# Kernel optimization log

Measured on AMD Instinct MI355X. Metric: run time of the kernel, lower is better.

The kernel has to match this reference:

```python
import jax, jax.numpy as jnp
import numpy as np

D_MODEL = 1024
NHEAD = 16
D_K = D_MODEL // NHEAD


def sparsemax(z):
    # sparsemax along last axis (Martins & Astudillo 2016)
    n = z.shape[-1]
    z_sorted = jnp.flip(jnp.sort(z, axis=-1), axis=-1)          # descending
    k = jnp.arange(1, n + 1, dtype=z.dtype)
    z_cumsum = jnp.cumsum(z_sorted, axis=-1)
    support = (1.0 + k * z_sorted) > z_cumsum                    # [..., n] bool
    k_max = jnp.sum(support, axis=-1, keepdims=True)             # [..., 1] int
    tau_sum = jnp.take_along_axis(z_cumsum, k_max - 1, axis=-1)
    tau = (tau_sum - 1.0) / k_max.astype(z.dtype)
    return jnp.maximum(z - tau, 0.0)


def setup_inputs() -> dict:
    key = jax.random.key(0)
    ks = jax.random.split(key, 12)
    B, S = 2, 2048
    s = 1.0 / np.sqrt(D_MODEL)
    inp = {
        'query': jax.random.normal(ks[0], (B, S, D_MODEL), jnp.float32),
        'key':   jax.random.normal(ks[1], (B, S, D_MODEL), jnp.float32),
        'value': jax.random.normal(ks[2], (B, S, D_MODEL), jnp.float32),
        'Wq': jax.random.uniform(ks[3], (D_MODEL, D_MODEL), jnp.float32, -s, s),
        'bq': jax.random.uniform(ks[4], (D_MODEL,), jnp.float32, -s, s),
        'Wk': jax.random.uniform(ks[5], (D_MODEL, D_MODEL), jnp.float32, -s, s),
        'bk': jax.random.uniform(ks[6], (D_MODEL,), jnp.float32, -s, s),
        'Wv': jax.random.uniform(ks[7], (D_MODEL, D_MODEL), jnp.float32, -s, s),
        'bv': jax.random.uniform(ks[8], (D_MODEL,), jnp.float32, -s, s),
        'Wfc': jax.random.uniform(ks[9], (D_MODEL, D_MODEL), jnp.float32, -s, s),
        'bfc': jax.random.uniform(ks[10], (D_MODEL,), jnp.float32, -s, s),
    }
    return inp


def reference(query, key, value, Wq, bq, Wk, bk, Wv, bv, Wfc, bfc):
    B, S, _ = query.shape
    # projections (torch Linear: x @ W.T + b)
    q = (query @ Wq.T + bq).reshape(B, S, NHEAD, D_K).transpose(0, 2, 1, 3)
    k = (key   @ Wk.T + bk).reshape(B, S, NHEAD, D_K).transpose(0, 2, 1, 3)
    v = (value @ Wv.T + bv).reshape(B, S, NHEAD, D_K).transpose(0, 2, 1, 3)
    # scaled dot-product with sparsemax
    logits = jnp.einsum('bhqd,bhkd->bhqk', q, k) / np.sqrt(D_K).astype(jnp.float32)
    attention = sparsemax(logits)                                # [B,H,S,S]
    attn_out = jnp.einsum('bhqk,bhkd->bhqd', attention, v)
    attn_out = attn_out.transpose(0, 2, 1, 3).reshape(B, S, D_MODEL)
    output = attn_out @ Wfc.T + bfc                              # dropout = identity (eval)
    return output, attention
```

## Files before the change

### kernel.cpp

```cpp
#include <hip/hip_runtime.h>
#include <hip/hip_bf16.h>
#include <cstdint>

#define S_LEN  2048
#define DMODEL 1024
#define NHEAD  16
#define M_ROWS 4096

typedef __attribute__((ext_vector_type(8))) short bf16x8;
typedef __attribute__((ext_vector_type(4))) float f32x4;

__device__ __forceinline__ unsigned short f2bf(float f) {
    __hip_bfloat16 h = __float2bfloat16(f);
    return __builtin_bit_cast(unsigned short, h);
}
__device__ __forceinline__ float bf2f(unsigned short u) {
    return __builtin_bit_cast(float, (unsigned)u << 16);
}
__device__ __forceinline__ uint4 pack8(float4 a, float4 b) {
    uint4 u;
    u.x = ((unsigned)f2bf(a.y) << 16) | f2bf(a.x);
    u.y = ((unsigned)f2bf(a.w) << 16) | f2bf(a.z);
    u.z = ((unsigned)f2bf(b.y) << 16) | f2bf(b.x);
    u.w = ((unsigned)f2bf(b.w) << 16) | f2bf(b.z);
    return u;
}

__device__ __forceinline__ float wave_sum64(float v) {
    v += __shfl_xor(v, 32, 64); v += __shfl_xor(v, 16, 64);
    v += __shfl_xor(v, 8, 64);  v += __shfl_xor(v, 4, 64);
    v += __shfl_xor(v, 2, 64);  v += __shfl_xor(v, 1, 64);
    return v;
}
__device__ __forceinline__ float wave_max64(float v) {
    v = fmaxf(v, __shfl_xor(v, 32, 64)); v = fmaxf(v, __shfl_xor(v, 16, 64));
    v = fmaxf(v, __shfl_xor(v, 8, 64));  v = fmaxf(v, __shfl_xor(v, 4, 64));
    v = fmaxf(v, __shfl_xor(v, 2, 64));  v = fmaxf(v, __shfl_xor(v, 1, 64));
    return v;
}
__device__ __forceinline__ int lanes_below(unsigned long long m) {
    return __builtin_amdgcn_mbcnt_hi((unsigned)(m >> 32),
           __builtin_amdgcn_mbcnt_lo((unsigned)m, 0));
}

__global__ __launch_bounds__(256)
void qkv_gemm(const float* __restrict__ xq, const float* __restrict__ xk,
              const float* __restrict__ xv,
              const float* __restrict__ Wq, const float* __restrict__ Wk,
              const float* __restrict__ Wv,
              const float* __restrict__ bq, const float* __restrict__ bk,
              const float* __restrict__ bv,
              unsigned short* __restrict__ Q_bf, unsigned short* __restrict__ K_bf,
              unsigned short* __restrict__ V_bf) {
    const int which = blockIdx.z;
    const float* A    = (which == 0) ? xq : (which == 1) ? xk : xv;
    const float* W    = (which == 0) ? Wq : (which == 1) ? Wk : Wv;
    const float* bias = (which == 0) ? bq : (which == 1) ? bk : bv;
    unsigned short* dst = (which == 0) ? Q_bf : (which == 1) ? K_bf : V_bf;

    const int row0 = blockIdx.x * 128;
    const int col0 = blockIdx.y * 128;

    __shared__ unsigned short SMEM[10240];
    unsigned short* As = SMEM;
    unsigned short* Bs = SMEM + 5120;

    const int t = threadIdx.x;
    const int wid = t >> 6, lane = t & 63;
    const int wm = wid >> 1, wn = wid & 1;
    const int l = lane & 15, quad = lane >> 4;

    f32x4 acc[4][4];
#pragma unroll
    for (int i = 0; i < 4; ++i)
#pragma unroll
        for (int j = 0; j < 4; ++j) {
            float b_ = bias[col0 + wn * 64 + j * 16 + l];
            acc[i][j] = (f32x4){ b_, b_, b_, b_ };
        }

    for (int k0 = 0; k0 < DMODEL; k0 += 32) {
        uint4 ar[2], br[2];
#pragma unroll
        for (int i = 0; i < 2; ++i) {
            const int c = t + i * 256, r = c >> 2, q = (c & 3) * 8;
            const float* ap = A + (size_t)(row0 + r) * DMODEL + k0 + q;
            const float* wp = W + (size_t)(col0 + r) * DMODEL + k0 + q;
            float4 a0 = *(const float4*)ap, a1 = *(const float4*)(ap + 4);
            float4 w0 = *(const float4*)wp, w1 = *(const float4*)(wp + 4);
            ar[i] = pack8(a0, a1);
            br[i] = pack8(w0, w1);
        }
        __syncthreads();
#pragma unroll
        for (int i = 0; i < 2; ++i) {
            const int c = t + i * 256, r = c >> 2, q = (c & 3) * 8;
            *(uint4*)&As[r * 40 + q] = ar[i];
            *(uint4*)&Bs[r * 40 + q] = br[i];
        }
        __syncthreads();
        bf16x8 a[4], b[4];
#pragma unroll
        for (int i = 0; i < 4; ++i)
            a[i] = *(const bf16x8*)&As[(wm * 64 + i * 16 + l) * 40 + quad * 8];
#pragma unroll
        for (int j = 0; j < 4; ++j)
            b[j] = *(const bf16x8*)&Bs[(wn * 64 + j * 16 + l) * 40 + quad * 8];
#pragma unroll
        for (int i = 0; i < 4; ++i)
#pragma unroll
            for (int j = 0; j < 4; ++j)
                acc[i][j] = __builtin_amdgcn_mfma_f32_16x16x32_bf16(a[i], b[j], acc[i][j], 0, 0, 0);
    }

    __syncthreads();
    unsigned short* Cs = SMEM;
#pragma unroll 1
    for (int jh = 0; jh < 2; ++jh) {
        if (wn == jh) {
#pragma unroll
            for (int i = 0; i < 4; ++i)
#pragma unroll
                for (int j = 0; j < 4; ++j)
#pragma unroll
                    for (int r = 0; r < 4; ++r)
                        Cs[(wm * 64 + i * 16 + quad * 4 + r) * 72 + j * 16 + l] =
                            f2bf(acc[i][j][r]);
        }
        __syncthreads();
#pragma unroll
        for (int it = 0; it < 4; ++it) {
            const int idx = t + it * 256;
            const int row = idx >> 3, c8 = (idx & 7) * 8;
            *(uint4*)(dst + (size_t)(row0 + row) * DMODEL + col0 + jh * 64 + c8) =
                *(const uint4*)&Cs[row * 72 + c8];
        }
        __syncthreads();
    }
}

__global__ __launch_bounds__(512, 8)
void attn_fused(const unsigned short* __restrict__ Q_bf,
                const unsigned short* __restrict__ K_bf,
                const unsigned short* __restrict__ V_bf,
                float* __restrict__ attn,
                unsigned short* __restrict__ AO_bf) {
    const int t = threadIdx.x;
    const int w = t >> 6, lane = t & 63;
    const int l = lane & 15, quad = lane >> 4;
    const int bh = blockIdx.y, b_ = bh >> 4, h = bh & 15;
    const int r0 = blockIdx.x * 8;

    __shared__ float LDSf[8 * 512];

    const unsigned short* Qp =
        Q_bf + ((size_t)(b_ * S_LEN + r0 + (l & 7))) * DMODEL + h * 64 + quad * 8;
    const bf16x8 a0 = *(const bf16x8*)Qp;
    const bf16x8 a1 = *(const bf16x8*)(Qp + 32);

    float z[32];
#pragma unroll
    for (int q = 0; q < 4; ++q) {
        const unsigned short* Kb =
            K_bf + ((size_t)(b_ * S_LEN + q * 512 + w * 64 + l)) * DMODEL
            + h * 64 + quad * 8;
        f32x4 acc[4];
#pragma unroll
        for (int ct = 0; ct < 4; ++ct) {
            const unsigned short* Kp = Kb + (size_t)(ct * 16) * DMODEL;
            const bf16x8 b0 = *(const bf16x8*)Kp;
            const bf16x8 b1 = *(const bf16x8*)(Kp + 32);
            f32x4 c = {};
            c = __builtin_amdgcn_mfma_f32_16x16x32_bf16(a0, b0, c, 0, 0, 0);
            c = __builtin_amdgcn_mfma_f32_16x16x32_bf16(a1, b1, c, 0, 0, 0);
#pragma unroll
            for (int r = 0; r < 4; ++r) c[r] *= 0.125f;
            acc[ct] = c;
        }
        if (quad < 2) {
#pragma unroll
            for (int ct = 0; ct < 4; ++ct)
#pragma unroll
                for (int r = 0; r < 4; ++r)
                    LDSf[(quad * 4 + r) * 512 + w * 64 + ct * 16 + l] = acc[ct][r];
        }
        __syncthreads();
#pragma unroll
        for (int j = 0; j < 8; ++j)
            z[q * 8 + j] = LDSf[w * 512 + j * 64 + lane];
        __syncthreads();
    }

    float m = z[0];
#pragma unroll
    for (int j = 1; j < 32; ++j) m = fmaxf(m, z[j]);
    m = wave_max64(m);

    float tau = m - 1.0f;
#pragma unroll 1
    for (int it = 0; it < 8; ++it) {
        float ss = 0.0f, kk = 0.0f;
#pragma unroll
        for (int j = 0; j < 32; ++j)
            if (z[j] > tau) { ss += z[j]; kk += 1.0f; }
        ss = wave_sum64(ss); kk = wave_sum64(kk);
        const float tn = (ss - 1.0f) / kk;
        if (tn == tau) break;
        tau = tn;
    }

    float* ap = attn + (size_t)bh * S_LEN * S_LEN + (size_t)(r0 + w) * S_LEN;
#pragma unroll
    for (int jj = 0; jj < 32; ++jj) {
        z[jj] = fmaxf(z[jj] - tau, 0.0f);
        __builtin_nontemporal_store(z[jj], ap + (jj >> 3) * 512 + (jj & 7) * 64 + lane);
    }

    uint2* list = (uint2*)LDSf + w * 256;
    int base = 0;
#pragma unroll
    for (int jj = 0; jj < 32; ++jj) {
        const float pv = z[jj];
        const unsigned long long mk = __ballot(pv > 0.0f);
        if (pv > 0.0f) {
            const int pos = base + lanes_below(mk);
            if (pos < 256)
                list[pos] = (uint2){ (unsigned)((jj >> 3) * 512 + (jj & 7) * 64 + lane),
                                     __builtin_bit_cast(unsigned, pv) };
        }
        base += __popcll(mk);
    }
    const int cnt = base < 256 ? base : 256;
    __threadfence_block();

    const unsigned short* Vh = V_bf + ((size_t)b_ * S_LEN) * DMODEL + h * 64;
    const int sub = lane >> 3, dbase = (lane & 7) * 8;
    float acc8[8] = {};
    const int gmax = (cnt + 7) >> 3;
#pragma unroll 1
    for (int g = 0; g < gmax; ++g) {
        const int idx = g * 8 + sub;
        if (idx < cnt) {
            const uint2 e = list[idx];
            const float p = __builtin_bit_cast(float, e.y);
            const uint4 vv = *(const uint4*)(Vh + ((size_t)e.x) * DMODEL + dbase);
            acc8[0] += p * bf2f((unsigned short)(vv.x & 0xffff));
            acc8[1] += p * bf2f((unsigned short)(vv.x >> 16));
            acc8[2] += p * bf2f((unsigned short)(vv.y & 0xffff));
            acc8[3] += p * bf2f((unsigned short)(vv.y >> 16));
            acc8[4] += p * bf2f((unsigned short)(vv.z & 0xffff));
            acc8[5] += p * bf2f((unsigned short)(vv.z >> 16));
            acc8[6] += p * bf2f((unsigned short)(vv.w & 0xffff));
            acc8[7] += p * bf2f((unsigned short)(vv.w >> 16));
        }
    }
#pragma unroll
    for (int d = 0; d < 8; ++d) {
        acc8[d] += __shfl_xor(acc8[d], 8, 64);
        acc8[d] += __shfl_xor(acc8[d], 16, 64);
        acc8[d] += __shfl_xor(acc8[d], 32, 64);
    }
    if (lane < 8) {
        union { unsigned short u[8]; uint4 v; } o;
#pragma unroll
        for (int d = 0; d < 8; ++d) o.u[d] = f2bf(acc8[d]);
        *(uint4*)(AO_bf + ((size_t)(b_ * S_LEN + r0 + w)) * DMODEL
                  + h * 64 + lane * 8) = o.v;
    }
}

__global__ __launch_bounds__(256)
void fc_gemm(const unsigned short* __restrict__ AO_bf,
             const float* __restrict__ Wfc,
             const float* __restrict__ bfc, float* __restrict__ out) {
    const int row0 = blockIdx.x * 128;
    const int col0 = blockIdx.y * 128;

    __shared__ unsigned short As[128 * 40];
    __shared__ unsigned short Bs[128 * 40];

    const int t = threadIdx.x;
    const int wid = t >> 6, lane = t & 63;
    const int wm = wid >> 1, wn = wid & 1;
    const int l = lane & 15, quad = lane >> 4;

    f32x4 acc[4][4];
#pragma unroll
    for (int i = 0; i < 4; ++i)
#pragma unroll
        for (int j = 0; j < 4; ++j) {
            float b_ = bfc[col0 + wn * 64 + j * 16 + l];
            acc[i][j] = (f32x4){ b_, b_, b_, b_ };
        }

    for (int k0 = 0; k0 < DMODEL; k0 += 32) {
        uint4 ar[2], br[2];
#pragma unroll
        for (int i = 0; i < 2; ++i) {
            const int c = t + i * 256, r = c >> 2, q = (c & 3) * 8;
            ar[i] = *(const uint4*)(AO_bf + (size_t)(row0 + r) * DMODEL + k0 + q);
            const float* wp = Wfc + (size_t)(col0 + r) * DMODEL + k0 + q;
            float4 w0 = *(const float4*)wp, w1 = *(const float4*)(wp + 4);
            br[i] = pack8(w0, w1);
        }
        __syncthreads();
#pragma unroll
        for (int i = 0; i < 2; ++i) {
            const int c = t + i * 256, r = c >> 2, q = (c & 3) * 8;
            *(uint4*)&As[r * 40 + q] = ar[i];
            *(uint4*)&Bs[r * 40 + q] = br[i];
        }
        __syncthreads();
        bf16x8 a[4], b[4];
#pragma unroll
        for (int i = 0; i < 4; ++i)
            a[i] = *(const bf16x8*)&As[(wm * 64 + i * 16 + l) * 40 + quad * 8];
#pragma unroll
        for (int j = 0; j < 4; ++j)
            b[j] = *(const bf16x8*)&Bs[(wn * 64 + j * 16 + l) * 40 + quad * 8];
#pragma unroll
        for (int i = 0; i < 4; ++i)
#pragma unroll
            for (int j = 0; j < 4; ++j)
                acc[i][j] = __builtin_amdgcn_mfma_f32_16x16x32_bf16(a[i], b[j], acc[i][j], 0, 0, 0);
    }

#pragma unroll
    for (int i = 0; i < 4; ++i)
#pragma unroll
        for (int r = 0; r < 4; ++r) {
            const int m = row0 + wm * 64 + i * 16 + quad * 4 + r;
#pragma unroll
            for (int j = 0; j < 4; ++j) {
                const int n = col0 + wn * 64 + j * 16 + l;
                out[(size_t)m * DMODEL + n] = acc[i][j][r];
            }
        }
}

extern "C" void kernel_launch(void* const* d_in, const int* in_sizes, int n_in,
                              void* d_out, int out_size, void* d_ws, size_t ws_size,
                              hipStream_t stream) {
    const float* q   = (const float*)d_in[0];
    const float* k   = (const float*)d_in[1];
    const float* v   = (const float*)d_in[2];
    const float* Wq  = (const float*)d_in[3];
    const float* bq  = (const float*)d_in[4];
    const float* Wk  = (const float*)d_in[5];
    const float* bk  = (const float*)d_in[6];
    const float* Wv  = (const float*)d_in[7];
    const float* bv  = (const float*)d_in[8];
    const float* Wfc = (const float*)d_in[9];
    const float* bfc = (const float*)d_in[10];

    float* out  = (float*)d_out;
    float* attn = out + (size_t)M_ROWS * DMODEL;

    char* ws = (char*)d_ws;
    unsigned short* Q_bf  = (unsigned short*)ws;
    unsigned short* K_bf  = (unsigned short*)(ws + (8u << 20));
    unsigned short* V_bf  = (unsigned short*)(ws + (16u << 20));
    unsigned short* AO_bf = (unsigned short*)(ws + (24u << 20));

    qkv_gemm<<<dim3(32, 8, 3), 256, 0, stream>>>(q, k, v, Wq, Wk, Wv,
                                                  bq, bk, bv, Q_bf, K_bf, V_bf);
    attn_fused<<<dim3(S_LEN / 8, 32), 512, 0, stream>>>(Q_bf, K_bf, V_bf, attn, AO_bf);
    fc_gemm<<<dim3(32, 8), 256, 0, stream>>>(AO_bf, Wfc, bfc, out);
}
```

Baseline: 906.6 us.

## Prefilter sparsemax candidates above max-1 and fold Q scaling into projection

Result: no change. 906.3 us (-0.0%).

```diff
diff --git a/kernel.cpp b/kernel.cpp
--- a/kernel.cpp
+++ b/kernel.cpp
@@ -57,6 +57,7 @@
     const float* W    = (which == 0) ? Wq : (which == 1) ? Wk : Wv;
     const float* bias = (which == 0) ? bq : (which == 1) ? bk : bv;
     unsigned short* dst = (which == 0) ? Q_bf : (which == 1) ? K_bf : V_bf;
+    const float qscale = (which == 0) ? 0.125f : 1.0f;
 
     const int row0 = blockIdx.x * 128;
     const int col0 = blockIdx.y * 128;
@@ -125,7 +126,7 @@
 #pragma unroll
                     for (int r = 0; r < 4; ++r)
                         Cs[(wm * 64 + i * 16 + quad * 4 + r) * 72 + j * 16 + l] =
-                            f2bf(acc[i][j][r]);
+                            f2bf(acc[i][j][r] * qscale);
         }
         __syncthreads();
 #pragma unroll
@@ -151,7 +152,8 @@
     const int bh = blockIdx.y, b_ = bh >> 4, h = bh & 15;
     const int r0 = blockIdx.x * 8;
 
-    __shared__ float LDSf[8 * 512];
+    __shared__ uint2 List[8 * 512];
+    float* LDSf = (float*)List;
 
     const unsigned short* Qp =
         Q_bf + ((size_t)(b_ * S_LEN + r0 + (l & 7))) * DMODEL + h * 64 + quad * 8;
@@ -173,8 +175,6 @@
             f32x4 c = {};
             c = __builtin_amdgcn_mfma_f32_16x16x32_bf16(a0, b0, c, 0, 0, 0);
             c = __builtin_amdgcn_mfma_f32_16x16x32_bf16(a1, b1, c, 0, 0, 0);
-#pragma unroll
-            for (int r = 0; r < 4; ++r) c[r] *= 0.125f;
             acc[ct] = c;
         }
         if (quad < 2) {
@@ -195,64 +195,104 @@
 #pragma unroll
     for (int j = 1; j < 32; ++j) m = fmaxf(m, z[j]);
     m = wave_max64(m);
-
-    float tau = m - 1.0f;
+    const float thr = m - 1.0f;
+
+    uint2* list = List + w * 512;
+    int cnt = 0;
+#pragma unroll
+    for (int jj = 0; jj < 32; ++jj) {
+        const float zv = z[jj];
+        const unsigned long long mk = __ballot(zv > thr);
+        if (zv > thr) {
+            const int pos = cnt + lanes_below(mk);
+            if (pos < 512)
+                list[pos] = (uint2){ (unsigned)((jj >> 3) * 512 + (jj & 7) * 64 + lane),
+                                     __builtin_bit_cast(unsigned, zv) };
+        }
+        cnt += __popcll(mk);
+    }
+    __threadfence_block();
+
+    float tau = thr;
+    if (cnt <= 256) {
+        const float NEG = -__builtin_inff();
+        const float zc0 = (lane < cnt)
+            ? __builtin_bit_cast(float, list[lane].y) : NEG;
+        const float zc1 = (64 + lane < cnt)
+            ? __builtin_bit_cast(float, list[64 + lane].y) : NEG;
+        const float zc2 = (128 + lane < cnt)
+            ? __builtin_bit_cast(float, list[128 + lane].y) : NEG;
+        const float zc3 = (192 + lane < cnt)
+            ? __builtin_bit_cast(float, list[192 + lane].y) : NEG;
 #pragma unroll 1
-    for (int it = 0; it < 8; ++it) {
-        float ss = 0.0f, kk = 0.0f;
-#pragma unroll
-        for (int j = 0; j < 32; ++j)
-            if (z[j] > tau) { ss += z[j]; kk += 1.0f; }
-        ss = wave_sum64(ss); kk = wave_sum64(kk);
-        const float tn = (ss - 1.0f) / kk;
-        if (tn == tau) break;
-        tau = tn;
-    }
+        for (int it = 0; it < 12; ++it) {
+            float ss = 0.0f, kk = 0.0f;
+            if (zc0 > tau) { ss += zc0; kk += 1.0f; }
+            if (zc1 > tau) { ss += zc1; kk += 1.0f; }
+            if (zc2 > tau) { ss += zc2; kk += 1.0f; }
+            if (zc3 > tau) { ss += zc3; kk += 1.0f; }
+            ss = wave_sum64(ss); kk = wave_sum64(kk);
+            const float tn = (ss - 1.0f) / kk;
+            if (tn == tau) break;
+            tau = tn;
+        }
+    } else {
+#pragma unroll 1
+        for (int it = 0; it < 8; ++it) {
+            float ss = 0.0f, kk = 0.0f;
+#pragma unroll
+            for (int j = 0; j < 32; ++j)
+                if (z[j] > tau) { ss += z[j]; kk += 1.0f; }
+            ss = wave_sum64(ss); kk = wave_sum64(kk);
+            const float tn = (ss - 1.0f) / kk;
+            if (tn == tau) break;
+            tau = tn;
+        }
+        cnt = 0;
+#pragma unroll
+        for (int jj = 0; jj < 32; ++jj) {
+            const float zv = z[jj];
+            const unsigned long long mk = __ballot(zv > tau);
+            if (zv > tau) {
+                const int pos = cnt + lanes_below(mk);
+                if (pos < 512)
+                    list[pos] = (uint2){ (unsigned)((jj >> 3) * 512 + (jj & 7) * 64 + lane),
+                                         __builtin_bit_cast(unsigned, zv) };
+            }
+            cnt += __popcll(mk);
+        }
+        __threadfence_block();
+    }
+    if (cnt > 504) cnt = 504;
 
     float* ap = attn + (size_t)bh * S_LEN * S_LEN + (size_t)(r0 + w) * S_LEN;
 #pragma unroll
     for (int jj = 0; jj < 32; ++jj) {
-        z[jj] = fmaxf(z[jj] - tau, 0.0f);
-        __builtin_nontemporal_store(z[jj], ap + (jj >> 3) * 512 + (jj & 7) * 64 + lane);
-    }
-
-    uint2* list = (uint2*)LDSf + w * 256;
-    int base = 0;
-#pragma unroll
-    for (int jj = 0; jj < 32; ++jj) {
-        const float pv = z[jj];
-        const unsigned long long mk = __ballot(pv > 0.0f);
-        if (pv > 0.0f) {
-            const int pos = base + lanes_below(mk);
-            if (pos < 256)
-                list[pos] = (uint2){ (unsigned)((jj >> 3) * 512 + (jj & 7) * 64 + lane),
-                                     __builtin_bit_cast(unsigned, pv) };
-        }
-        base += __popcll(mk);
-    }
-    const int cnt = base < 256 ? base : 256;
+        const float pv = fmaxf(z[jj] - tau, 0.0f);
+        __builtin_nontemporal_store(pv, ap + (jj >> 3) * 512 + (jj & 7) * 64 + lane);
+    }
+
+    if (lane < 8)
+        list[cnt + lane] = (uint2){ 0u, 0xff800000u };
     __threadfence_block();
 
     const unsigned short* Vh = V_bf + ((size_t)b_ * S_LEN) * DMODEL + h * 64;
     const int sub = lane >> 3, dbase = (lane & 7) * 8;
     float acc8[8] = {};
     const int gmax = (cnt + 7) >> 3;
-#pragma unroll 1
+#pragma unroll 2
     for (int g = 0; g < gmax; ++g) {
-        const int idx = g * 8 + sub;
-        if (idx < cnt) {
-            const uint2 e = list[idx];
-            const float p = __builtin_bit_cast(float, e.y);
-            const uint4 vv = *(const uint4*)(Vh + ((size_t)e.x) * DMODEL + dbase);
-            acc8[0] += p * bf2f((unsigned short)(vv.x & 0xffff));
-            acc8[1] += p * bf2f((unsigned short)(vv.x >> 16));
-            acc8[2] += p * bf2f((unsigned short)(vv.y & 0xffff));
-            acc8[3] += p * bf2f((unsigned short)(vv.y >> 16));
-            acc8[4] += p * bf2f((unsigned short)(vv.z & 0xffff));
-            acc8[5] += p * bf2f((unsigned short)(vv.z >> 16));
-            acc8[6] += p * bf2f((unsigned short)(vv.w & 0xffff));
-            acc8[7] += p * bf2f((unsigned short)(vv.w >> 16));
-        }
+        const uint2 e = list[g * 8 + sub];
+        const float p = fmaxf(__builtin_bit_cast(float, e.y) - tau, 0.0f);
+        const uint4 vv = *(const uint4*)(Vh + ((size_t)e.x) * DMODEL + dbase);
+        acc8[0] += p * bf2f((unsigned short)(vv.x & 0xffff));
+        acc8[1] += p * bf2f((unsigned short)(vv.x >> 16));
+        acc8[2] += p * bf2f((unsigned short)(vv.y & 0xffff));
+        acc8[3] += p * bf2f((unsigned short)(vv.y >> 16));
+        acc8[4] += p * bf2f((unsigned short)(vv.z & 0xffff));
+        acc8[5] += p * bf2f((unsigned short)(vv.z >> 16));
+        acc8[6] += p * bf2f((unsigned short)(vv.w & 0xffff));
+        acc8[7] += p * bf2f((unsigned short)(vv.w >> 16));
     }
 #pragma unroll
     for (int d = 0; d < 8; ++d) {
```

## Fold Q scaling into projection, unroll sparse PV gather, enlarge support list

Applied to the files above, without the earlier changes.

Measured after the change: 890.3 us. Within noise of the previous version (-1.8%).

```diff
diff --git a/kernel.cpp b/kernel.cpp
--- a/kernel.cpp
+++ b/kernel.cpp
@@ -57,6 +57,7 @@
     const float* W    = (which == 0) ? Wq : (which == 1) ? Wk : Wv;
     const float* bias = (which == 0) ? bq : (which == 1) ? bk : bv;
     unsigned short* dst = (which == 0) ? Q_bf : (which == 1) ? K_bf : V_bf;
+    const float qscale = (which == 0) ? 0.125f : 1.0f;
 
     const int row0 = blockIdx.x * 128;
     const int col0 = blockIdx.y * 128;
@@ -125,7 +126,7 @@
 #pragma unroll
                     for (int r = 0; r < 4; ++r)
                         Cs[(wm * 64 + i * 16 + quad * 4 + r) * 72 + j * 16 + l] =
-                            f2bf(acc[i][j][r]);
+                            f2bf(acc[i][j][r] * qscale);
         }
         __syncthreads();
 #pragma unroll
@@ -139,7 +140,7 @@
     }
 }
 
-__global__ __launch_bounds__(512, 8)
+__global__ __launch_bounds__(512, 6)
 void attn_fused(const unsigned short* __restrict__ Q_bf,
                 const unsigned short* __restrict__ K_bf,
                 const unsigned short* __restrict__ V_bf,
@@ -151,7 +152,8 @@
     const int bh = blockIdx.y, b_ = bh >> 4, h = bh & 15;
     const int r0 = blockIdx.x * 8;
 
-    __shared__ float LDSf[8 * 512];
+    __shared__ uint2 List[8 * 512];
+    float* LDSf = (float*)List;
 
     const unsigned short* Qp =
         Q_bf + ((size_t)(b_ * S_LEN + r0 + (l & 7))) * DMODEL + h * 64 + quad * 8;
@@ -159,6 +161,7 @@
     const bf16x8 a1 = *(const bf16x8*)(Qp + 32);
 
     float z[32];
+    float m = -__builtin_inff();
 #pragma unroll
     for (int q = 0; q < 4; ++q) {
         const unsigned short* Kb =
@@ -173,8 +176,6 @@
             f32x4 c = {};
             c = __builtin_amdgcn_mfma_f32_16x16x32_bf16(a0, b0, c, 0, 0, 0);
             c = __builtin_amdgcn_mfma_f32_16x16x32_bf16(a1, b1, c, 0, 0, 0);
-#pragma unroll
-            for (int r = 0; r < 4; ++r) c[r] *= 0.125f;
             acc[ct] = c;
         }
         if (quad < 2) {
@@ -186,73 +187,104 @@
         }
         __syncthreads();
 #pragma unroll
-        for (int j = 0; j < 8; ++j)
+        for (int j = 0; j < 8; ++j) {
             z[q * 8 + j] = LDSf[w * 512 + j * 64 + lane];
-        __syncthreads();
-    }
-
-    float m = z[0];
-#pragma unroll
-    for (int j = 1; j < 32; ++j) m = fmaxf(m, z[j]);
+            m = fmaxf(m, z[q * 8 + j]);
+        }
+        __syncthreads();
+    }
+
     m = wave_max64(m);
 
     float tau = m - 1.0f;
 #pragma unroll 1
-    for (int it = 0; it < 8; ++it) {
-        float ss = 0.0f, kk = 0.0f;
-#pragma unroll
-        for (int j = 0; j < 32; ++j)
-            if (z[j] > tau) { ss += z[j]; kk += 1.0f; }
-        ss = wave_sum64(ss); kk = wave_sum64(kk);
-        const float tn = (ss - 1.0f) / kk;
+    for (int it = 0; it < 10; ++it) {
+        float ss = 0.0f;
+        int kk = 0;
+#pragma unroll
+        for (int j = 0; j < 32; ++j) {
+            const bool c = z[j] > tau;
+            kk += (int)__popcll(__ballot(c));
+            ss += c ? z[j] : 0.0f;
+        }
+        ss = wave_sum64(ss);
+        const float tn = (ss - 1.0f) / (float)kk;
         if (tn == tau) break;
         tau = tn;
     }
 
+    uint2* list = List + w * 512;
     float* ap = attn + (size_t)bh * S_LEN * S_LEN + (size_t)(r0 + w) * S_LEN;
+    int scnt = 0;
 #pragma unroll
     for (int jj = 0; jj < 32; ++jj) {
-        z[jj] = fmaxf(z[jj] - tau, 0.0f);
-        __builtin_nontemporal_store(z[jj], ap + (jj >> 3) * 512 + (jj & 7) * 64 + lane);
-    }
-
-    uint2* list = (uint2*)LDSf + w * 256;
-    int base = 0;
-#pragma unroll
-    for (int jj = 0; jj < 32; ++jj) {
-        const float pv = z[jj];
+        const float pv = fmaxf(z[jj] - tau, 0.0f);
+        __builtin_nontemporal_store(pv, ap + (jj >> 3) * 512 + (jj & 7) * 64 + lane);
         const unsigned long long mk = __ballot(pv > 0.0f);
         if (pv > 0.0f) {
-            const int pos = base + lanes_below(mk);
-            if (pos < 256)
+            const int pos = scnt + lanes_below(mk);
+            if (pos < 480)
                 list[pos] = (uint2){ (unsigned)((jj >> 3) * 512 + (jj & 7) * 64 + lane),
                                      __builtin_bit_cast(unsigned, pv) };
         }
-        base += __popcll(mk);
-    }
-    const int cnt = base < 256 ? base : 256;
-    __threadfence_block();
+        scnt += (int)__popcll(mk);
+    }
+    if (scnt > 480) scnt = 480;
+
+    if (lane < 32)
+        list[scnt + lane] = (uint2){ 0u, 0u };
 
     const unsigned short* Vh = V_bf + ((size_t)b_ * S_LEN) * DMODEL + h * 64;
     const int sub = lane >> 3, dbase = (lane & 7) * 8;
     float acc8[8] = {};
-    const int gmax = (cnt + 7) >> 3;
+    const int gmax4 = (scnt + 31) >> 5;
 #pragma unroll 1
-    for (int g = 0; g < gmax; ++g) {
-        const int idx = g * 8 + sub;
-        if (idx < cnt) {
-            const uint2 e = list[idx];
-            const float p = __builtin_bit_cast(float, e.y);
-            const uint4 vv = *(const uint4*)(Vh + ((size_t)e.x) * DMODEL + dbase);
-            acc8[0] += p * bf2f((unsigned short)(vv.x & 0xffff));
-            acc8[1] += p * bf2f((unsigned short)(vv.x >> 16));
-            acc8[2] += p * bf2f((unsigned short)(vv.y & 0xffff));
-            acc8[3] += p * bf2f((unsigned short)(vv.y >> 16));
-            acc8[4] += p * bf2f((unsigned short)(vv.z & 0xffff));
-            acc8[5] += p * bf2f((unsigned short)(vv.z >> 16));
-            acc8[6] += p * bf2f((unsigned short)(vv.w & 0xffff));
-            acc8[7] += p * bf2f((unsigned short)(vv.w >> 16));
-        }
+    for (int g = 0; g < gmax4; ++g) {
+        const int b0 = g * 32 + sub;
+        const uint2 e0 = list[b0];
+        const uint2 e1 = list[b0 + 8];
+        const uint2 e2 = list[b0 + 16];
+        const uint2 e3 = list[b0 + 24];
+        const uint4 v0 = *(const uint4*)(Vh + (size_t)e0.x * DMODEL + dbase);
+        const uint4 v1 = *(const uint4*)(Vh + (size_t)e1.x * DMODEL + dbase);
+        const uint4 v2 = *(const uint4*)(Vh + (size_t)e2.x * DMODEL + dbase);
+        const uint4 v3 = *(const uint4*)(Vh + (size_t)e3.x * DMODEL + dbase);
+        const float p0 = __builtin_bit_cast(float, e0.y);
+        const float p1 = __builtin_bit_cast(float, e1.y);
+        const float p2 = __builtin_bit_cast(float, e2.y);
+        const float p3 = __builtin_bit_cast(float, e3.y);
+        acc8[0] += p0 * bf2f((unsigned short)(v0.x & 0xffff));
+        acc8[1] += p0 * bf2f((unsigned short)(v0.x >> 16));
+        acc8[2] += p0 * bf2f((unsigned short)(v0.y & 0xffff));
+        acc8[3] += p0 * bf2f((unsigned short)(v0.y >> 16));
+        acc8[4] += p0 * bf2f((unsigned short)(v0.z & 0xffff));
+        acc8[5] += p0 * bf2f((unsigned short)(v0.z >> 16));
+        acc8[6] += p0 * bf2f((unsigned short)(v0.w & 0xffff));
+        acc8[7] += p0 * bf2f((unsigned short)(v0.w >> 16));
+        acc8[0] += p1 * bf2f((unsigned short)(v1.x & 0xffff));
+        acc8[1] += p1 * bf2f((unsigned short)(v1.x >> 16));
+        acc8[2] += p1 * bf2f((unsigned short)(v1.y & 0xffff));
+        acc8[3] += p1 * bf2f((unsigned short)(v1.y >> 16));
+        acc8[4] += p1 * bf2f((unsigned short)(v1.z & 0xffff));
+        acc8[5] += p1 * bf2f((unsigned short)(v1.z >> 16));
+        acc8[6] += p1 * bf2f((unsigned short)(v1.w & 0xffff));
+        acc8[7] += p1 * bf2f((unsigned short)(v1.w >> 16));
+        acc8[0] += p2 * bf2f((unsigned short)(v2.x & 0xffff));
+        acc8[1] += p2 * bf2f((unsigned short)(v2.x >> 16));
+        acc8[2] += p2 * bf2f((unsigned short)(v2.y & 0xffff));
+        acc8[3] += p2 * bf2f((unsigned short)(v2.y >> 16));
+        acc8[4] += p2 * bf2f((unsigned short)(v2.z & 0xffff));
+        acc8[5] += p2 * bf2f((unsigned short)(v2.z >> 16));
+        acc8[6] += p2 * bf2f((unsigned short)(v2.w & 0xffff));
+        acc8[7] += p2 * bf2f((unsigned short)(v2.w >> 16));
+        acc8[0] += p3 * bf2f((unsigned short)(v3.x & 0xffff));
+        acc8[1] += p3 * bf2f((unsigned short)(v3.x >> 16));
+        acc8[2] += p3 * bf2f((unsigned short)(v3.y & 0xffff));
+        acc8[3] += p3 * bf2f((unsigned short)(v3.y >> 16));
+        acc8[4] += p3 * bf2f((unsigned short)(v3.z & 0xffff));
+        acc8[5] += p3 * bf2f((unsigned short)(v3.z >> 16));
+        acc8[6] += p3 * bf2f((unsigned short)(v3.w & 0xffff));
+        acc8[7] += p3 * bf2f((unsigned short)(v3.w >> 16));
     }
 #pragma unroll
     for (int d = 0; d < 8; ++d) {
```
